# Kernel tuning notes

Measured on AMD Instinct MI355X. Metric: run time of the kernel, lower is better.

The kernel has to match this reference:

```python
import jax, jax.numpy as jnp
import numpy as np

N, E = 50000, 800000
IN, HID, HEADS, OUT = 128, 64, 4, 32


def _lin_init(key, fin, fout):
    k1, k2 = jax.random.split(key)
    W = jax.random.normal(k1, (fin, fout), jnp.float32) / np.float32(np.sqrt(fin))
    b = jax.random.normal(k2, (fout,), jnp.float32) * 0.01
    return W, b


def setup_inputs() -> dict:
    key = jax.random.key(0)
    ks = jax.random.split(key, 12)
    x = jax.random.normal(ks[0], (N, IN), jnp.float32)
    edge_index = jax.random.randint(ks[1], (2, E), 0, N, dtype=jnp.int32)
    Wq1, bq1 = _lin_init(ks[2], IN, HEADS * HID)
    Wk1, bk1 = _lin_init(ks[3], IN, HEADS * HID)
    Wv1, bv1 = _lin_init(ks[4], IN, HEADS * HID)
    Ws1, bs1 = _lin_init(ks[5], IN, HID)  # skip: concat=False -> in -> hidden
    Wq2, bq2 = _lin_init(ks[6], HID, HEADS * HID)
    Wk2, bk2 = _lin_init(ks[7], HID, HEADS * HID)
    Wv2, bv2 = _lin_init(ks[8], HID, HEADS * HID)
    Ws2, bs2 = _lin_init(ks[9], HID, HID)
    ln_g = jnp.ones((HID,), jnp.float32)
    ln_b = jnp.zeros((HID,), jnp.float32)
    Wf, bf = _lin_init(ks[10], HID, OUT)
    return dict(x=x, edge_index=edge_index,
                Wq1=Wq1, bq1=bq1, Wk1=Wk1, bk1=bk1, Wv1=Wv1, bv1=bv1, Ws1=Ws1, bs1=bs1,
                Wq2=Wq2, bq2=bq2, Wk2=Wk2, bk2=bk2, Wv2=Wv2, bv2=bv2, Ws2=Ws2, bs2=bs2,
                ln_g=ln_g, ln_b=ln_b, Wf=Wf, bf=bf)


def transformer_conv(x, src, dst, Wq, bq, Wk, bk, Wv, bv, Ws, bs):
    """PyG TransformerConv, heads=HEADS, concat=False (head-mean), root_weight=True."""
    n = x.shape[0]
    q = (x @ Wq + bq).reshape(n, HEADS, HID)
    k = (x @ Wk + bk).reshape(n, HEADS, HID)
    v = (x @ Wv + bv).reshape(n, HEADS, HID)
    # per-edge attention logits: query at target (dst), key at source (src)
    logits = jnp.einsum('ehd,ehd->eh', q[dst], k[src]) / np.float32(np.sqrt(HID))  # [E,H]
    m = jax.ops.segment_max(logits, dst, num_segments=n)          # [N,H]
    e = jnp.exp(logits - m[dst])
    s = jax.ops.segment_sum(e, dst, num_segments=n)               # [N,H]
    alpha = e / s[dst]                                            # segment softmax
    agg = jax.ops.segment_sum(alpha[:, :, None] * v[src], dst, num_segments=n)  # [N,H,D]
    return agg.mean(axis=1) + (x @ Ws + bs)


def layernorm(x, g, b):
    mu = x.mean(-1, keepdims=True)
    var = x.var(-1, keepdims=True)
    return (x - mu) / jnp.sqrt(var + 1e-5) * g + b


def reference(x, edge_index, Wq1, bq1, Wk1, bk1, Wv1, bv1, Ws1, bs1,
              Wq2, bq2, Wk2, bk2, Wv2, bv2, Ws2, bs2, ln_g, ln_b, Wf, bf):
    src, dst = edge_index[0], edge_index[1]
    h = transformer_conv(x, src, dst, Wq1, bq1, Wk1, bk1, Wv1, bv1, Ws1, bs1)
    h = jax.nn.relu(layernorm(h, ln_g, ln_b))  # dropout = identity (eval)
    h = transformer_conv(h, src, dst, Wq2, bq2, Wk2, bk2, Wv2, bv2, Ws2, bs2)
    h = layernorm(h, ln_g, ln_b)  # k == num_layers-2: no relu/dropout
    return h @ Wf + bf
```

## Files before the change

### kernel.cpp

```cpp
#include <hip/hip_runtime.h>
#include <hip/hip_fp16.h>
#include <math.h>

#define NN 50000
#define EE 800000
#define HEADS 4
#define HIDD 64
#define OUTF 32

struct __align__(8)  h4v { __half2 a, b; };
struct __align__(16) h8v { __half2 a, b, c, d; };

typedef __attribute__((ext_vector_type(8))) _Float16 f16x8;
typedef __attribute__((ext_vector_type(4))) _Float16 f16x4;
typedef __attribute__((ext_vector_type(4))) float    f32x4;

template<int KDIM>
__global__ __launch_bounds__(256) void qkvs_gemm(
    const float* __restrict__ X,
    const float* __restrict__ Wq, const float* __restrict__ bq,
    const float* __restrict__ Wk, const float* __restrict__ bk,
    const float* __restrict__ Wv, const float* __restrict__ bv,
    const float* __restrict__ Ws, const float* __restrict__ bs,
    float* __restrict__ Q, __half* __restrict__ KV, float* __restrict__ SKP)
{
    constexpr int KP = KDIM + 8;
    __shared__ _Float16 Asm[64 * KP];
    __shared__ _Float16 Bsm[64 * KP];

    const int nwg = gridDim.x;
    const int i   = blockIdx.x;
    const int q8  = nwg >> 3, r8 = nwg & 7;
    const int xcd = i & 7, j = i >> 3;
    const int w   = (xcd < r8 ? xcd * (q8 + 1) : r8 * (q8 + 1) + (xcd - r8) * q8) + j;

    const int nt   = w % 13;
    const int row0 = (w / 13) * 64;

    const float* W; const float* bias; int mode, bcol, wstride;
    if (nt < 4)       { W = Wq; bias = bq; mode = 0; bcol = nt*64;     wstride = 256; }
    else if (nt < 8)  { W = Wk; bias = bk; mode = 1; bcol = (nt-4)*64; wstride = 256; }
    else if (nt < 12) { W = Wv; bias = bv; mode = 2; bcol = (nt-8)*64; wstride = 256; }
    else              { W = Ws; bias = bs; mode = 3; bcol = 0;         wstride = 64;  }

    const int tid = threadIdx.x;

    constexpr int AF4 = 64 * KDIM / 4;
    #pragma unroll
    for (int li = tid; li < AF4; li += 256) {
        int r = li / (KDIM/4), c4 = li % (KDIM/4);
        int gr = row0 + r;
        float4 a4 = {0.f,0.f,0.f,0.f};
        if (gr < NN) a4 = *(const float4*)&X[(size_t)gr*KDIM + c4*4];
        f16x4 hv = { (_Float16)a4.x, (_Float16)a4.y, (_Float16)a4.z, (_Float16)a4.w };
        *(f16x4*)&Asm[r*KP + c4*4] = hv;
    }
    constexpr int BF4 = KDIM * 16;
    #pragma unroll
    for (int li = tid; li < BF4; li += 256) {
        int k = li >> 4, c4 = li & 15;
        float4 wv4 = *(const float4*)&W[(size_t)k*wstride + bcol + c4*4];
        Bsm[(c4*4+0)*KP + k] = (_Float16)wv4.x;
        Bsm[(c4*4+1)*KP + k] = (_Float16)wv4.y;
        Bsm[(c4*4+2)*KP + k] = (_Float16)wv4.z;
        Bsm[(c4*4+3)*KP + k] = (_Float16)wv4.w;
    }
    __syncthreads();

    const int lane = tid & 63, wvi = tid >> 6;
    const int lr = lane & 15, lg = lane >> 4;
    const int arow = wvi*16 + lr;

    f32x4 acc[4];
    #pragma unroll
    for (int ci = 0; ci < 4; ++ci) acc[ci] = (f32x4){0.f,0.f,0.f,0.f};

    #pragma unroll
    for (int k0 = 0; k0 < KDIM; k0 += 32) {
        f16x8 af = *(const f16x8*)&Asm[arow*KP + k0 + lg*8];
        #pragma unroll
        for (int ci = 0; ci < 4; ++ci) {
            f16x8 bf = *(const f16x8*)&Bsm[(ci*16 + lr)*KP + k0 + lg*8];
            acc[ci] = __builtin_amdgcn_mfma_f32_16x16x32_f16(af, bf, acc[ci], 0, 0, 0);
        }
    }

    #pragma unroll
    for (int ci = 0; ci < 4; ++ci) {
        const int col = ci*16 + lr;
        const float bia = bias[bcol + col];
        #pragma unroll
        for (int ii = 0; ii < 4; ++ii) {
            int gr = row0 + wvi*16 + lg*4 + ii;
            if (gr >= NN) continue;
            float o = acc[ci][ii] + bia;
            if (mode == 0) {
                Q[(size_t)gr*256 + bcol + col] = o;
            } else if (mode == 3) {
                SKP[(size_t)gr*64 + col] = o;
            } else {
                int h = bcol >> 6;
                int d = col;
                size_t idx = (size_t)gr*512 + h*128 + ((d>>2)<<3) + (d&3)
                             + (mode == 2 ? 4 : 0);
                KV[idx] = __float2half(o);
            }
        }
    }
}

__global__ __launch_bounds__(256) void hist_kernel(const int* __restrict__ dstA,
                                                   int* __restrict__ deg)
{
    int e = blockIdx.x * 256 + threadIdx.x;
    atomicAdd(&deg[dstA[e]], 1);
}

__global__ __launch_bounds__(1024) void scan_kernel(const int* __restrict__ deg,
                                                    int* __restrict__ rowptr,
                                                    int* __restrict__ cursor)
{
    __shared__ int sdata[1024];
    __shared__ int soff;
    const int tid = threadIdx.x;
    if (tid == 0) soff = 0;
    __syncthreads();
    for (int base = 0; base < NN; base += 1024) {
        int v = (base + tid < NN) ? deg[base + tid] : 0;
        sdata[tid] = v;
        __syncthreads();
        #pragma unroll
        for (int off = 1; off < 1024; off <<= 1) {
            int t = (tid >= off) ? sdata[tid - off] : 0;
            __syncthreads();
            sdata[tid] += t;
            __syncthreads();
        }
        int excl = sdata[tid] - v;
        if (base + tid < NN) {
            rowptr[base + tid] = soff + excl;
            cursor[base + tid] = soff + excl;
        }
        int total = sdata[1023];
        __syncthreads();
        if (tid == 0) soff += total;
        __syncthreads();
    }
    if (tid == 0) rowptr[NN] = EE;
}

__global__ __launch_bounds__(256) void scatter_kernel(const int* __restrict__ srcA,
                                                      const int* __restrict__ dstA,
                                                      int* __restrict__ cursor,
                                                      int* __restrict__ colidx)
{
    int e = blockIdx.x * 256 + threadIdx.x;
    int p = atomicAdd(&cursor[dstA[e]], 1);
    colidx[p] = srcA[e];
}

template<bool RELU>
__global__ __launch_bounds__(256) void node_attn(
    const int* __restrict__ rowptr, const int* __restrict__ colidx,
    const float* __restrict__ Q, const __half* __restrict__ KV,
    const float* __restrict__ SKP,
    const float* __restrict__ g, const float* __restrict__ b,
    float* __restrict__ Hout)
{
    int n = (blockIdx.x * blockDim.x + threadIdx.x) >> 6;
    if (n >= NN) return;
    const int lane = threadIdx.x & 63;
    const int h = lane >> 4, t = lane & 15;
    const int kvoff = h*128 + t*8;

    const float4 q4 = *(const float4*)&Q[(size_t)n*256 + h*64 + t*4];

    float4 acc = {0.f,0.f,0.f,0.f};
    float ssum = 0.f;
    const int e0 = rowptr[n], e1 = rowptr[n+1];
    int e = e0;
    for (; e + 2 <= e1; e += 2) {
        const int s0 = colidx[e], s1 = colidx[e+1];
        const h8v kv0 = *(const h8v*)&KV[(size_t)s0*512 + kvoff];
        const h8v kv1 = *(const h8v*)&KV[(size_t)s1*512 + kvoff];
        const float2 k0a = __half22float2(kv0.a), k0b = __half22float2(kv0.b);
        const float2 k1a = __half22float2(kv1.a), k1b = __half22float2(kv1.b);
        float p0 = q4.x*k0a.x + q4.y*k0a.y + q4.z*k0b.x + q4.w*k0b.y;
        float p1 = q4.x*k1a.x + q4.y*k1a.y + q4.z*k1b.x + q4.w*k1b.y;
        p0 += __shfl_xor(p0, 1);  p1 += __shfl_xor(p1, 1);
        p0 += __shfl_xor(p0, 2);  p1 += __shfl_xor(p1, 2);
        p0 += __shfl_xor(p0, 4);  p1 += __shfl_xor(p1, 4);
        p0 += __shfl_xor(p0, 8);  p1 += __shfl_xor(p1, 8);
        const float eh0 = __expf(p0 * 0.125f);
        const float eh1 = __expf(p1 * 0.125f);
        const float2 v0a = __half22float2(kv0.c), v0b = __half22float2(kv0.d);
        const float2 v1a = __half22float2(kv1.c), v1b = __half22float2(kv1.d);
        ssum  += eh0 + eh1;
        acc.x += eh0*v0a.x + eh1*v1a.x;
        acc.y += eh0*v0a.y + eh1*v1a.y;
        acc.z += eh0*v0b.x + eh1*v1b.x;
        acc.w += eh0*v0b.y + eh1*v1b.y;
    }
    for (; e < e1; ++e) {
        const int s = colidx[e];
        const h8v kv = *(const h8v*)&KV[(size_t)s*512 + kvoff];
        const float2 ka = __half22float2(kv.a), kb = __half22float2(kv.b);
        float p = q4.x*ka.x + q4.y*ka.y + q4.z*kb.x + q4.w*kb.y;
        p += __shfl_xor(p, 1);
        p += __shfl_xor(p, 2);
        p += __shfl_xor(p, 4);
        p += __shfl_xor(p, 8);
        const float eh = __expf(p * 0.125f);
        const float2 va = __half22float2(kv.c), vb = __half22float2(kv.d);
        ssum  += eh;
        acc.x += eh*va.x; acc.y += eh*va.y; acc.z += eh*vb.x; acc.w += eh*vb.y;
    }
    const float inv = (ssum != 0.f) ? 1.f/ssum : 0.f;
    acc.x *= inv; acc.y *= inv; acc.z *= inv; acc.w *= inv;

    #pragma unroll
    for (int o = 16; o < 64; o <<= 1) {
        acc.x += __shfl_xor(acc.x, o); acc.y += __shfl_xor(acc.y, o);
        acc.z += __shfl_xor(acc.z, o); acc.w += __shfl_xor(acc.w, o);
    }
    const float4 sk4 = *(const float4*)&SKP[(size_t)n*64 + t*4];
    float4 val;
    val.x = acc.x*0.25f + sk4.x; val.y = acc.y*0.25f + sk4.y;
    val.z = acc.z*0.25f + sk4.z; val.w = acc.w*0.25f + sk4.w;

    float m  = val.x + val.y + val.z + val.w;
    float m2 = val.x*val.x + val.y*val.y + val.z*val.z + val.w*val.w;
    #pragma unroll
    for (int o = 1; o < 16; o <<= 1) { m += __shfl_xor(m, o); m2 += __shfl_xor(m2, o); }
    m *= (1.f/64.f); m2 *= (1.f/64.f);
    const float rstd = rsqrtf(m2 - m*m + 1e-5f);
    const float4 g4 = *(const float4*)&g[t*4];
    const float4 b4 = *(const float4*)&b[t*4];
    float4 y;
    y.x = (val.x - m)*rstd*g4.x + b4.x;
    y.y = (val.y - m)*rstd*g4.y + b4.y;
    y.z = (val.z - m)*rstd*g4.z + b4.z;
    y.w = (val.w - m)*rstd*g4.w + b4.w;
    if (RELU) {
        y.x = fmaxf(y.x, 0.f); y.y = fmaxf(y.y, 0.f);
        y.z = fmaxf(y.z, 0.f); y.w = fmaxf(y.w, 0.f);
    }
    if (h == 0) *(float4*)&Hout[(size_t)n*64 + t*4] = y;
}

__global__ __launch_bounds__(256) void final_gemm(
    const float* __restrict__ H, const float* __restrict__ Wf,
    const float* __restrict__ bf, float* __restrict__ out)
{
    __shared__ float sW[64][32];
    __shared__ float sH[8][64];
    const int tid = threadIdx.x;
    #pragma unroll
    for (int i = 0; i < 8; ++i) {
        int li = tid + 256*i;
        sW[li >> 5][li & 31] = Wf[li];
    }
    const int n0 = blockIdx.x * 8;
    #pragma unroll
    for (int i = 0; i < 2; ++i) {
        int li = tid + 256*i;
        int r = li >> 6, d = li & 63;
        int gn = n0 + r;
        sH[r][d] = (gn < NN) ? H[(size_t)gn*64 + d] : 0.f;
    }
    __syncthreads();
    const int o = tid & 31, nl = tid >> 5;
    const int gn = n0 + nl;
    if (gn >= NN) return;
    float acc = bf[o];
    #pragma unroll
    for (int dd = 0; dd < 64; ++dd) acc += sH[nl][dd] * sW[dd][o];
    out[(size_t)gn*32 + o] = acc;
}

extern "C" void kernel_launch(void* const* d_in, const int* in_sizes, int n_in,
                              void* d_out, int out_size, void* d_ws, size_t ws_size,
                              hipStream_t stream) {
    const float* x   = (const float*)d_in[0];
    const int*   ei  = (const int*)d_in[1];
    const int* srcA = ei;
    const int* dstA = ei + EE;
    const float *Wq1=(const float*)d_in[2],  *bq1=(const float*)d_in[3];
    const float *Wk1=(const float*)d_in[4],  *bk1=(const float*)d_in[5];
    const float *Wv1=(const float*)d_in[6],  *bv1=(const float*)d_in[7];
    const float *Ws1=(const float*)d_in[8],  *bs1=(const float*)d_in[9];
    const float *Wq2=(const float*)d_in[10], *bq2=(const float*)d_in[11];
    const float *Wk2=(const float*)d_in[12], *bk2=(const float*)d_in[13];
    const float *Wv2=(const float*)d_in[14], *bv2=(const float*)d_in[15];
    const float *Ws2=(const float*)d_in[16], *bs2=(const float*)d_in[17];
    const float *ln_g=(const float*)d_in[18],*ln_b=(const float*)d_in[19];
    const float *Wf=(const float*)d_in[20],  *bf=(const float*)d_in[21];
    float* out = (float*)d_out;

    float* ws = (float*)d_ws;
    size_t off = 0;
    float* Q    = ws + off; off += (size_t)NN*256;
    __half* KV  = (__half*)(ws + off); off += (size_t)NN*256;
    float* SKP  = ws + off; off += (size_t)NN*64;
    float* H1   = ws + off; off += (size_t)NN*64;
    float* H2   = ws + off; off += (size_t)NN*64;
    int* deg    = (int*)(ws + off); off += NN;
    int* rowptr = (int*)(ws + off); off += NN + 1;
    int* cursor = (int*)(ws + off); off += NN;
    int* colidx = (int*)(ws + off); off += EE;

    const int rowTiles  = (NN + 63) / 64;
    const int gemmGrid  = 13 * rowTiles;
    const int edgeBlocks = EE / 256;
    const int nodeBlocks = NN / 4;

    hipMemsetAsync(deg, 0, NN * sizeof(int), stream);
    hist_kernel<<<edgeBlocks, 256, 0, stream>>>(dstA, deg);
    scan_kernel<<<1, 1024, 0, stream>>>(deg, rowptr, cursor);
    scatter_kernel<<<edgeBlocks, 256, 0, stream>>>(srcA, dstA, cursor, colidx);

    qkvs_gemm<128><<<gemmGrid, 256, 0, stream>>>(x, Wq1,bq1, Wk1,bk1, Wv1,bv1, Ws1,bs1,
                                                 Q, KV, SKP);
    node_attn<true><<<nodeBlocks, 256, 0, stream>>>(rowptr, colidx, Q, KV, SKP,
                                                    ln_g, ln_b, H1);

    qkvs_gemm<64><<<gemmGrid, 256, 0, stream>>>(H1, Wq2,bq2, Wk2,bk2, Wv2,bv2, Ws2,bs2,
                                                Q, KV, SKP);
    node_attn<false><<<nodeBlocks, 256, 0, stream>>>(rowptr, colidx, Q, KV, SKP,
                                                     ln_g, ln_b, H2);

    final_gemm<<<NN / 8, 256, 0, stream>>>(H2, Wf, bf, out);
}
```

Baseline: 688.7 us.

## Pre-convert GEMM inputs to fp16 and read MFMA operands directly from global

Adds prep kernels that convert x to padded fp16 and transpose all weight matrices to fp16 once per call. The QKV/skip GEMM then drops its shared-memory staging and loads MFMA fragments straight from global memory. The node attention kernels now write their hidden outputs in fp16, which halves the traffic into the second GEMM and the final projection. In exchange there are ten extra small launches, uncached global fragment loads in the GEMM, and slightly lower precision for the hidden states.

```diff
diff --git a/kernel.cpp b/kernel.cpp
--- a/kernel.cpp
+++ b/kernel.cpp
@@ -4,6 +4,7 @@
 
 #define NN 50000
 #define EE 800000
+#define NPAD 50048
 #define HEADS 4
 #define HIDD 64
 #define OUTF 32
@@ -15,19 +16,43 @@
 typedef __attribute__((ext_vector_type(4))) _Float16 f16x4;
 typedef __attribute__((ext_vector_type(4))) float    f32x4;
 
+__global__ __launch_bounds__(256) void prep_x(const float* __restrict__ X,
+                                              _Float16* __restrict__ Xh)
+{
+    int li = blockIdx.x * 256 + threadIdx.x;
+    if (li >= NPAD * 32) return;
+    int r = li >> 5, c4 = li & 31;
+    float4 a4 = {0.f, 0.f, 0.f, 0.f};
+    if (r < NN) a4 = *(const float4*)&X[(size_t)r * 128 + c4 * 4];
+    f16x4 hv = { (_Float16)a4.x, (_Float16)a4.y, (_Float16)a4.z, (_Float16)a4.w };
+    *(f16x4*)&Xh[(size_t)r * 128 + c4 * 4] = hv;
+}
+
+__global__ __launch_bounds__(256) void transpose_w(const float* __restrict__ src,
+                                                   _Float16* __restrict__ dst,
+                                                   int K, int COLS)
+{
+    int idx = blockIdx.x * 256 + threadIdx.x;
+    if (idx >= K * COLS) return;
+    int k = idx / COLS, col = idx % COLS;
+    dst[(size_t)col * K + k] = (_Float16)src[idx];
+}
+
+__global__ __launch_bounds__(256) void pad_h(_Float16* __restrict__ Hh)
+{
+    int idx = blockIdx.x * 256 + threadIdx.x;
+    if (idx >= (NPAD - NN) * 64) return;
+    Hh[(size_t)NN * 64 + idx] = (_Float16)0.f;
+}
+
 template<int KDIM>
 __global__ __launch_bounds__(256) void qkvs_gemm(
-    const float* __restrict__ X,
-    const float* __restrict__ Wq, const float* __restrict__ bq,
-    const float* __restrict__ Wk, const float* __restrict__ bk,
-    const float* __restrict__ Wv, const float* __restrict__ bv,
-    const float* __restrict__ Ws, const float* __restrict__ bs,
+    const _Float16* __restrict__ A,
+    const _Float16* __restrict__ WT,
+    const float* __restrict__ bq, const float* __restrict__ bk,
+    const float* __restrict__ bv, const float* __restrict__ bs,
     float* __restrict__ Q, __half* __restrict__ KV, float* __restrict__ SKP)
 {
-    constexpr int KP = KDIM + 8;
-    __shared__ _Float16 Asm[64 * KP];
-    __shared__ _Float16 Bsm[64 * KP];
-
     const int nwg = gridDim.x;
     const int i   = blockIdx.x;
     const int q8  = nwg >> 3, r8 = nwg & 7;
@@ -37,71 +62,49 @@
     const int nt   = w % 13;
     const int row0 = (w / 13) * 64;
 
-    const float* W; const float* bias; int mode, bcol, wstride;
-    if (nt < 4)       { W = Wq; bias = bq; mode = 0; bcol = nt*64;     wstride = 256; }
-    else if (nt < 8)  { W = Wk; bias = bk; mode = 1; bcol = (nt-4)*64; wstride = 256; }
-    else if (nt < 12) { W = Wv; bias = bv; mode = 2; bcol = (nt-8)*64; wstride = 256; }
-    else              { W = Ws; bias = bs; mode = 3; bcol = 0;         wstride = 64;  }
+    const float* bias; int mode, bcol;
+    if (nt < 4)       { bias = bq; mode = 0; bcol = nt * 64; }
+    else if (nt < 8)  { bias = bk; mode = 1; bcol = (nt - 4) * 64; }
+    else if (nt < 12) { bias = bv; mode = 2; bcol = (nt - 8) * 64; }
+    else              { bias = bs; mode = 3; bcol = 0; }
+    const _Float16* WTt = WT + ((size_t)mode * 256 + bcol) * KDIM;
 
     const int tid = threadIdx.x;
-
-    constexpr int AF4 = 64 * KDIM / 4;
-    #pragma unroll
-    for (int li = tid; li < AF4; li += 256) {
-        int r = li / (KDIM/4), c4 = li % (KDIM/4);
-        int gr = row0 + r;
-        float4 a4 = {0.f,0.f,0.f,0.f};
-        if (gr < NN) a4 = *(const float4*)&X[(size_t)gr*KDIM + c4*4];
-        f16x4 hv = { (_Float16)a4.x, (_Float16)a4.y, (_Float16)a4.z, (_Float16)a4.w };
-        *(f16x4*)&Asm[r*KP + c4*4] = hv;
-    }
-    constexpr int BF4 = KDIM * 16;
-    #pragma unroll
-    for (int li = tid; li < BF4; li += 256) {
-        int k = li >> 4, c4 = li & 15;
-        float4 wv4 = *(const float4*)&W[(size_t)k*wstride + bcol + c4*4];
-        Bsm[(c4*4+0)*KP + k] = (_Float16)wv4.x;
-        Bsm[(c4*4+1)*KP + k] = (_Float16)wv4.y;
-        Bsm[(c4*4+2)*KP + k] = (_Float16)wv4.z;
-        Bsm[(c4*4+3)*KP + k] = (_Float16)wv4.w;
-    }
-    __syncthreads();
-
     const int lane = tid & 63, wvi = tid >> 6;
     const int lr = lane & 15, lg = lane >> 4;
-    const int arow = wvi*16 + lr;
+    const size_t arow = row0 + wvi * 16 + lr;
 
     f32x4 acc[4];
     #pragma unroll
-    for (int ci = 0; ci < 4; ++ci) acc[ci] = (f32x4){0.f,0.f,0.f,0.f};
+    for (int ci = 0; ci < 4; ++ci) acc[ci] = (f32x4){0.f, 0.f, 0.f, 0.f};
 
     #pragma unroll
     for (int k0 = 0; k0 < KDIM; k0 += 32) {
-        f16x8 af = *(const f16x8*)&Asm[arow*KP + k0 + lg*8];
+        f16x8 af = *(const f16x8*)&A[arow * KDIM + k0 + lg * 8];
         #pragma unroll
         for (int ci = 0; ci < 4; ++ci) {
-            f16x8 bf = *(const f16x8*)&Bsm[(ci*16 + lr)*KP + k0 + lg*8];
+            f16x8 bf = *(const f16x8*)&WTt[(size_t)(ci * 16 + lr) * KDIM + k0 + lg * 8];
             acc[ci] = __builtin_amdgcn_mfma_f32_16x16x32_f16(af, bf, acc[ci], 0, 0, 0);
         }
     }
 
     #pragma unroll
     for (int ci = 0; ci < 4; ++ci) {
-        const int col = ci*16 + lr;
+        const int col = ci * 16 + lr;
         const float bia = bias[bcol + col];
         #pragma unroll
         for (int ii = 0; ii < 4; ++ii) {
-            int gr = row0 + wvi*16 + lg*4 + ii;
+            int gr = row0 + wvi * 16 + lg * 4 + ii;
             if (gr >= NN) continue;
             float o = acc[ci][ii] + bia;
             if (mode == 0) {
-                Q[(size_t)gr*256 + bcol + col] = o;
+                Q[(size_t)gr * 256 + bcol + col] = o;
             } else if (mode == 3) {
-                SKP[(size_t)gr*64 + col] = o;
+                SKP[(size_t)gr * 64 + col] = o;
             } else {
                 int h = bcol >> 6;
                 int d = col;
-                size_t idx = (size_t)gr*512 + h*128 + ((d>>2)<<3) + (d&3)
+                size_t idx = (size_t)gr * 512 + h * 128 + ((d >> 2) << 3) + (d & 3)
                              + (mode == 2 ? 4 : 0);
                 KV[idx] = __float2half(o);
             }
@@ -165,28 +168,28 @@
     const float* __restrict__ Q, const __half* __restrict__ KV,
     const float* __restrict__ SKP,
     const float* __restrict__ g, const float* __restrict__ b,
-    float* __restrict__ Hout)
+    __half* __restrict__ Hout)
 {
     int n = (blockIdx.x * blockDim.x + threadIdx.x) >> 6;
     if (n >= NN) return;
     const int lane = threadIdx.x & 63;
     const int h = lane >> 4, t = lane & 15;
-    const int kvoff = h*128 + t*8;
-
-    const float4 q4 = *(const float4*)&Q[(size_t)n*256 + h*64 + t*4];
-
-    float4 acc = {0.f,0.f,0.f,0.f};
+    const int kvoff = h * 128 + t * 8;
+
+    const float4 q4 = *(const float4*)&Q[(size_t)n * 256 + h * 64 + t * 4];
+
+    float4 acc = {0.f, 0.f, 0.f, 0.f};
     float ssum = 0.f;
-    const int e0 = rowptr[n], e1 = rowptr[n+1];
+    const int e0 = rowptr[n], e1 = rowptr[n + 1];
     int e = e0;
     for (; e + 2 <= e1; e += 2) {
-        const int s0 = colidx[e], s1 = colidx[e+1];
-        const h8v kv0 = *(const h8v*)&KV[(size_t)s0*512 + kvoff];
-        const h8v kv1 = *(const h8v*)&KV[(size_t)s1*512 + kvoff];
+        const int s0 = colidx[e], s1 = colidx[e + 1];
+        const h8v kv0 = *(const h8v*)&KV[(size_t)s0 * 512 + kvoff];
+        const h8v kv1 = *(const h8v*)&KV[(size_t)s1 * 512 + kvoff];
         const float2 k0a = __half22float2(kv0.a), k0b = __half22float2(kv0.b);
         const float2 k1a = __half22float2(kv1.a), k1b = __half22float2(kv1.b);
-        float p0 = q4.x*k0a.x + q4.y*k0a.y + q4.z*k0b.x + q4.w*k0b.y;
-        float p1 = q4.x*k1a.x + q4.y*k1a.y + q4.z*k1b.x + q4.w*k1b.y;
+        float p0 = q4.x * k0a.x + q4.y * k0a.y + q4.z * k0b.x + q4.w * k0b.y;
+        float p1 = q4.x * k1a.x + q4.y * k1a.y + q4.z * k1b.x + q4.w * k1b.y;
         p0 += __shfl_xor(p0, 1);  p1 += __shfl_xor(p1, 1);
         p0 += __shfl_xor(p0, 2);  p1 += __shfl_xor(p1, 2);
         p0 += __shfl_xor(p0, 4);  p1 += __shfl_xor(p1, 4);
@@ -196,16 +199,16 @@
         const float2 v0a = __half22float2(kv0.c), v0b = __half22float2(kv0.d);
         const float2 v1a = __half22float2(kv1.c), v1b = __half22float2(kv1.d);
         ssum  += eh0 + eh1;
-        acc.x += eh0*v0a.x + eh1*v1a.x;
-        acc.y += eh0*v0a.y + eh1*v1a.y;
-        acc.z += eh0*v0b.x + eh1*v1b.x;
-        acc.w += eh0*v0b.y + eh1*v1b.y;
+        acc.x += eh0 * v0a.x + eh1 * v1a.x;
+        acc.y += eh0 * v0a.y + eh1 * v1a.y;
+        acc.z += eh0 * v0b.x + eh1 * v1b.x;
+        acc.w += eh0 * v0b.y + eh1 * v1b.y;
     }
     for (; e < e1; ++e) {
         const int s = colidx[e];
-        const h8v kv = *(const h8v*)&KV[(size_t)s*512 + kvoff];
+        const h8v kv = *(const h8v*)&KV[(size_t)s * 512 + kvoff];
         const float2 ka = __half22float2(kv.a), kb = __half22float2(kv.b);
-        float p = q4.x*ka.x + q4.y*ka.y + q4.z*kb.x + q4.w*kb.y;
+        float p = q4.x * ka.x + q4.y * ka.y + q4.z * kb.x + q4.w * kb.y;
         p += __shfl_xor(p, 1);
         p += __shfl_xor(p, 2);
         p += __shfl_xor(p, 4);
@@ -213,9 +216,9 @@
         const float eh = __expf(p * 0.125f);
         const float2 va = __half22float2(kv.c), vb = __half22float2(kv.d);
         ssum  += eh;
-        acc.x += eh*va.x; acc.y += eh*va.y; acc.z += eh*vb.x; acc.w += eh*vb.y;
-    }
-    const float inv = (ssum != 0.f) ? 1.f/ssum : 0.f;
+        acc.x += eh * va.x; acc.y += eh * va.y; acc.z += eh * vb.x; acc.w += eh * vb.y;
+    }
+    const float inv = (ssum != 0.f) ? 1.f / ssum : 0.f;
     acc.x *= inv; acc.y *= inv; acc.z *= inv; acc.w *= inv;
 
     #pragma unroll
@@ -223,33 +226,38 @@
         acc.x += __shfl_xor(acc.x, o); acc.y += __shfl_xor(acc.y, o);
         acc.z += __shfl_xor(acc.z, o); acc.w += __shfl_xor(acc.w, o);
     }
-    const float4 sk4 = *(const float4*)&SKP[(size_t)n*64 + t*4];
+    const float4 sk4 = *(const float4*)&SKP[(size_t)n * 64 + t * 4];
     float4 val;
-    val.x = acc.x*0.25f + sk4.x; val.y = acc.y*0.25f + sk4.y;
-    val.z = acc.z*0.25f + sk4.z; val.w = acc.w*0.25f + sk4.w;
+    val.x = acc.x * 0.25f + sk4.x; val.y = acc.y * 0.25f + sk4.y;
+    val.z = acc.z * 0.25f + sk4.z; val.w = acc.w * 0.25f + sk4.w;
 
     float m  = val.x + val.y + val.z + val.w;
-    float m2 = val.x*val.x + val.y*val.y + val.z*val.z + val.w*val.w;
+    float m2 = val.x * val.x + val.y * val.y + val.z * val.z + val.w * val.w;
     #pragma unroll
     for (int o = 1; o < 16; o <<= 1) { m += __shfl_xor(m, o); m2 += __shfl_xor(m2, o); }
-    m *= (1.f/64.f); m2 *= (1.f/64.f);
-    const float rstd = rsqrtf(m2 - m*m + 1e-5f);
-    const float4 g4 = *(const float4*)&g[t*4];
-    const float4 b4 = *(const float4*)&b[t*4];
+    m *= (1.f / 64.f); m2 *= (1.f / 64.f);
+    const float rstd = rsqrtf(m2 - m * m + 1e-5f);
+    const float4 g4 = *(const float4*)&g[t * 4];
+    const float4 b4 = *(const float4*)&b[t * 4];
     float4 y;
-    y.x = (val.x - m)*rstd*g4.x + b4.x;
-    y.y = (val.y - m)*rstd*g4.y + b4.y;
-    y.z = (val.z - m)*rstd*g4.z + b4.z;
-    y.w = (val.w - m)*rstd*g4.w + b4.w;
+    y.x = (val.x - m) * rstd * g4.x + b4.x;
+    y.y = (val.y - m) * rstd * g4.y + b4.y;
+    y.z = (val.z - m) * rstd * g4.z + b4.z;
+    y.w = (val.w - m) * rstd * g4.w + b4.w;
     if (RELU) {
         y.x = fmaxf(y.x, 0.f); y.y = fmaxf(y.y, 0.f);
         y.z = fmaxf(y.z, 0.f); y.w = fmaxf(y.w, 0.f);
     }
-    if (h == 0) *(float4*)&Hout[(size_t)n*64 + t*4] = y;
+    if (h == 0) {
+        h4v hv;
+        hv.a = __floats2half2_rn(y.x, y.y);
+        hv.b = __floats2half2_rn(y.z, y.w);
+        *(h4v*)&Hout[(size_t)n * 64 + t * 4] = hv;
+    }
 }
 
 __global__ __launch_bounds__(256) void final_gemm(
-    const float* __restrict__ H, const float* __restrict__ Wf,
+    const __half* __restrict__ H, const float* __restrict__ Wf,
     const float* __restrict__ bf, float* __restrict__ out)
 {
     __shared__ float sW[64][32];
@@ -257,16 +265,16 @@
     const int tid = threadIdx.x;
     #pragma unroll
     for (int i = 0; i < 8; ++i) {
-        int li = tid + 256*i;
+        int li = tid + 256 * i;
         sW[li >> 5][li & 31] = Wf[li];
     }
     const int n0 = blockIdx.x * 8;
     #pragma unroll
     for (int i = 0; i < 2; ++i) {
-        int li = tid + 256*i;
+        int li = tid + 256 * i;
         int r = li >> 6, d = li & 63;
         int gn = n0 + r;
-        sH[r][d] = (gn < NN) ? H[(size_t)gn*64 + d] : 0.f;
+        sH[r][d] = (gn < NN) ? __half2float(H[(size_t)gn * 64 + d]) : 0.f;
     }
     __syncthreads();
     const int o = tid & 31, nl = tid >> 5;
@@ -275,7 +283,7 @@
     float acc = bf[o];
     #pragma unroll
     for (int dd = 0; dd < 64; ++dd) acc += sH[nl][dd] * sW[dd][o];
-    out[(size_t)gn*32 + o] = acc;
+    out[(size_t)gn * 32 + o] = acc;
 }
 
 extern "C" void kernel_launch(void* const* d_in, const int* in_sizes, int n_in,
@@ -299,35 +307,49 @@
 
     float* ws = (float*)d_ws;
     size_t off = 0;
-    float* Q    = ws + off; off += (size_t)NN*256;
-    __half* KV  = (__half*)(ws + off); off += (size_t)NN*256;
-    float* SKP  = ws + off; off += (size_t)NN*64;
-    float* H1   = ws + off; off += (size_t)NN*64;
-    float* H2   = ws + off; off += (size_t)NN*64;
+    float* Q      = ws + off; off += (size_t)NN * 256;
+    __half* KV    = (__half*)(ws + off); off += (size_t)NN * 256;
+    float* SKP    = ws + off; off += (size_t)NN * 64;
+    _Float16* Xh  = (_Float16*)(ws + off); off += (size_t)NPAD * 64;
+    __half* H1h   = (__half*)(ws + off); off += (size_t)NPAD * 32;
+    __half* H2h   = (__half*)(ws + off); off += (size_t)NPAD * 32;
+    _Float16* WT1 = (_Float16*)(ws + off); off += (832 * 128) / 2;
+    _Float16* WT2 = (_Float16*)(ws + off); off += (832 * 64) / 2;
     int* deg    = (int*)(ws + off); off += NN;
     int* rowptr = (int*)(ws + off); off += NN + 1;
     int* cursor = (int*)(ws + off); off += NN;
     int* colidx = (int*)(ws + off); off += EE;
 
-    const int rowTiles  = (NN + 63) / 64;
-    const int gemmGrid  = 13 * rowTiles;
+    const int rowTiles   = NPAD / 64;
+    const int gemmGrid   = 13 * rowTiles;
     const int edgeBlocks = EE / 256;
     const int nodeBlocks = NN / 4;
+
+    prep_x<<<(NPAD * 32 + 255) / 256, 256, 0, stream>>>(x, Xh);
+    transpose_w<<<(128 * 256 + 255) / 256, 256, 0, stream>>>(Wq1, WT1 + 0,            128, 256);
+    transpose_w<<<(128 * 256 + 255) / 256, 256, 0, stream>>>(Wk1, WT1 + 256 * 128,    128, 256);
+    transpose_w<<<(128 * 256 + 255) / 256, 256, 0, stream>>>(Wv1, WT1 + 512 * 128,    128, 256);
+    transpose_w<<<(128 * 64  + 255) / 256, 256, 0, stream>>>(Ws1, WT1 + 768 * 128,    128, 64);
+    transpose_w<<<(64 * 256  + 255) / 256, 256, 0, stream>>>(Wq2, WT2 + 0,            64, 256);
+    transpose_w<<<(64 * 256  + 255) / 256, 256, 0, stream>>>(Wk2, WT2 + 256 * 64,     64, 256);
+    transpose_w<<<(64 * 256  + 255) / 256, 256, 0, stream>>>(Wv2, WT2 + 512 * 64,     64, 256);
+    transpose_w<<<(64 * 64   + 255) / 256, 256, 0, stream>>>(Ws2, WT2 + 768 * 64,     64, 64);
+    pad_h<<<((NPAD - NN) * 64 + 255) / 256, 256, 0, stream>>>((_Float16*)H1h);
 
     hipMemsetAsync(deg, 0, NN * sizeof(int), stream);
     hist_kernel<<<edgeBlocks, 256, 0, stream>>>(dstA, deg);
     scan_kernel<<<1, 1024, 0, stream>>>(deg, rowptr, cursor);
     scatter_kernel<<<edgeBlocks, 256, 0, stream>>>(srcA, dstA, cursor, colidx);
 
-    qkvs_gemm<128><<<gemmGrid, 256, 0, stream>>>(x, Wq1,bq1, Wk1,bk1, Wv1,bv1, Ws1,bs1,
+    qkvs_gemm<128><<<gemmGrid, 256, 0, stream>>>(Xh, WT1, bq1, bk1, bv1, bs1,
                                                  Q, KV, SKP);
     node_attn<true><<<nodeBlocks, 256, 0, stream>>>(rowptr, colidx, Q, KV, SKP,
-                                                    ln_g, ln_b, H1);
-
-    qkvs_gemm<64><<<gemmGrid, 256, 0, stream>>>(H1, Wq2,bq2, Wk2,bk2, Wv2,bv2, Ws2,bs2,
-                                                Q, KV, SKP);
+                                                    ln_g, ln_b, H1h);
+
+    qkvs_gemm<64><<<gemmGrid, 256, 0, stream>>>((const _Float16*)H1h, WT2,
+                                                bq2, bk2, bv2, bs2, Q, KV, SKP);
     node_attn<false><<<nodeBlocks, 256, 0, stream>>>(rowptr, colidx, Q, KV, SKP,
-                                                     ln_g, ln_b, H2);
-
-    final_gemm<<<NN / 8, 256, 0, stream>>>(H2, Wf, bf, out);
-}
+                                                     ln_g, ln_b, H2h);
+
+    final_gemm<<<NN / 8, 256, 0, stream>>>(H2h, Wf, bf, out);
+}
```

New measurement: 717.8 us. 1.04x slower.
